# Kernel optimization log

Measured on AMD Instinct MI355X. Metric: run time of the kernel, lower is better.

Reference implementation:

```python
import jax, jax.numpy as jnp
import numpy as np

N_NODES = 100000
N_EDGES = 1000000
N_GRAPHS = 2048
IN_DIM, HIDDEN, OUT_DIM = 5, 64, 128


def setup_inputs() -> dict:
    key = jax.random.key(0)
    ks = jax.random.split(key, 12)
    x = jax.random.normal(ks[0], (N_NODES, IN_DIM), dtype=jnp.float32)
    edge_index = jax.random.randint(ks[1], (2, N_EDGES), 0, N_NODES, dtype=jnp.int64)
    batch = jnp.sort(jax.random.randint(ks[2], (N_NODES,), 0, N_GRAPHS, dtype=jnp.int64))
    def lin(k, fan_in, fan_out):
        bound = 1.0 / np.sqrt(fan_in)
        kw, kb = jax.random.split(k)
        W = jax.random.uniform(kw, (fan_in, fan_out), jnp.float32, -bound, bound)
        b = jax.random.uniform(kb, (fan_out,), jnp.float32, -bound, bound)
        return W, b
    W1, b1 = lin(ks[3], IN_DIM, HIDDEN)
    W2, b2 = lin(ks[4], HIDDEN, HIDDEN)
    W3, b3 = lin(ks[5], HIDDEN, HIDDEN)
    W4, b4 = lin(ks[6], HIDDEN, OUT_DIM)
    return {"x": x, "edge_index": edge_index, "batch": batch,
            "W1": W1, "b1": b1, "W2": W2, "b2": b2,
            "W3": W3, "b3": b3, "W4": W4, "b4": b4}


def _gcn_conv(x, W, b, src, dst, norm, n):
    # h = x W; message from src, scaled by symmetric norm, scattered to dst
    h = x @ W                                   # [N, F]
    msg = h[src] * norm[:, None]                # [E+N, F] gather
    agg = jax.ops.segment_sum(msg, dst, num_segments=n)  # scatter-add
    return agg + b


def reference(x, edge_index, batch, W1, b1, W2, b2, W3, b3, W4, b4):
    n = x.shape[0]
    loop = jnp.arange(n, dtype=edge_index.dtype)
    # GCN with self-loops: src -> dst aggregation, D^-1/2 A_hat D^-1/2 norm
    src = jnp.concatenate([edge_index[0], loop])
    dst = jnp.concatenate([edge_index[1], loop])
    deg = jax.ops.segment_sum(jnp.ones_like(dst, dtype=x.dtype), dst, num_segments=n)
    dinv = jnp.where(deg > 0, jax.lax.rsqrt(jnp.maximum(deg, 1.0)), 0.0)
    norm = dinv[src] * dinv[dst]                # [E+N]

    h = jax.nn.relu(_gcn_conv(x, W1, b1, src, dst, norm, n))
    h = jax.nn.relu(_gcn_conv(h, W2, b2, src, dst, norm, n))

    # global mean pool per graph
    sums = jax.ops.segment_sum(h, batch, num_segments=N_GRAPHS)      # [G, F]
    cnts = jax.ops.segment_sum(jnp.ones((n,), h.dtype), batch, num_segments=N_GRAPHS)
    pooled = sums / jnp.maximum(cnts, 1.0)[:, None]

    # MLP head
    z = jax.nn.relu(pooled @ W3 + b3)
    return z @ W4 + b4
```

## Files before the change

### kernel.cpp

```cpp
#include <hip/hip_runtime.h>
#include <hip/hip_fp16.h>

#define N_NODES  100000
#define N_EDGES  1000000
#define N_GRAPHS 2048
#define IN_DIM   5
#define HIDDEN   64
#define OUT_DIM  128
#define CAP      32
#define NA       512
#define PART     256
#define NBIN     391
#define LSTR     72

typedef _Float16 f16x8 __attribute__((ext_vector_type(8)));
typedef float    f32x4 __attribute__((ext_vector_type(4)));

__global__ void k_hist(const int* __restrict__ dst, int* __restrict__ histT) {
    __shared__ int h[NBIN];
    int t = threadIdx.x, b = blockIdx.x;
    for (int i = t; i < NBIN; i += 256) h[i] = 0;
    __syncthreads();
    for (int e = b * 256 + t; e < N_EDGES; e += NA * 256)
        atomicAdd(&h[dst[e] >> 8], 1);
    __syncthreads();
    for (int i = t; i < NBIN; i += 256) histT[i * NA + b] = h[i];
}

__global__ void k_scanA(int* __restrict__ histT, int* __restrict__ total) {
    __shared__ int s[2][256];
    int bin = blockIdx.x, t = threadIdx.x;
    int* col = histT + bin * NA;
    int v0 = col[2 * t], v1 = col[2 * t + 1];
    int pair = v0 + v1;
    int cur = 0;
    s[0][t] = pair;
    __syncthreads();
    for (int off = 1; off < 256; off <<= 1) {
        int nv = s[cur][t] + ((t >= off) ? s[cur][t - off] : 0);
        s[cur ^ 1][t] = nv;
        cur ^= 1;
        __syncthreads();
    }
    int incl = s[cur][t];
    int excl = incl - pair;
    col[2 * t]     = excl;
    col[2 * t + 1] = excl + v0;
    if (t == 255) total[bin] = incl;
}

__global__ void k_scanB(const int* __restrict__ total, int* __restrict__ binBase) {
    __shared__ int s[2][512];
    int t = threadIdx.x;
    int v = (t < NBIN) ? total[t] : 0;
    int cur = 0;
    s[0][t] = v;
    __syncthreads();
    for (int off = 1; off < 512; off <<= 1) {
        int nv = s[cur][t] + ((t >= off) ? s[cur][t - off] : 0);
        s[cur ^ 1][t] = nv;
        cur ^= 1;
        __syncthreads();
    }
    if (t < NBIN) binBase[t] = s[cur][t] - v;
    if (t == NBIN - 1) binBase[NBIN] = s[cur][t];
}

__global__ void k_part(const int* __restrict__ src, const int* __restrict__ dst,
                       const int* __restrict__ histT, const int* __restrict__ binBase,
                       int* __restrict__ epart) {
    __shared__ int off[NBIN];
    int t = threadIdx.x, b = blockIdx.x;
    for (int i = t; i < NBIN; i += 256)
        off[i] = binBase[i] + histT[i * NA + b];
    __syncthreads();
    for (int e = b * 256 + t; e < N_EDGES; e += NA * 256) {
        int d = dst[e];
        int pos = atomicAdd(&off[d >> 8], 1);
        epart[pos] = ((d & (PART - 1)) << 17) | src[e];
    }
}

__global__ void __launch_bounds__(256) k_build(
        const int* __restrict__ epart, const int* __restrict__ binBase,
        const float* __restrict__ x, int* __restrict__ cnt, int* __restrict__ bkt,
        float* __restrict__ dinv, __half* __restrict__ xs) {
    __shared__ int lcnt[PART];
    __shared__ int lrows[PART * CAP];
    int t = threadIdx.x, b = blockIdx.x;
    int base = b * PART;
    for (int i = t; i < PART; i += 256) lcnt[i] = 0;
    __syncthreads();
    int estart = binBase[b], eend = binBase[b + 1];
    for (int i = estart + t; i < eend; i += 256) {
        int ed = epart[i];
        int ln = ed >> 17;
        int c = atomicAdd(&lcnt[ln], 1);
        if (c < CAP) lrows[ln * CAP + c] = ed & 0x1FFFF;
    }
    __syncthreads();
    int gbase = base * CAP;
    int lim = min(PART * CAP, N_NODES * CAP - gbase);
    for (int i = t; i < lim; i += 256) bkt[gbase + i] = lrows[i];
    for (int n = t; n < PART; n += 256) {
        int g = base + n;
        if (g < N_NODES) {
            int c = lcnt[n];
            cnt[g] = c;
            float d = rsqrtf(1.0f + (float)c);
            dinv[g] = d;
#pragma unroll
            for (int k = 0; k < 8; k++)
                xs[(size_t)g * 8 + k] =
                    __float2half((k < IN_DIM) ? x[g * IN_DIM + k] * d : 0.0f);
        }
    }
}

__global__ void __launch_bounds__(256) k_g5l12(
        const int* __restrict__ cnt, const int* __restrict__ bkt,
        const __half* __restrict__ xs,
        const float* __restrict__ W1, const float* __restrict__ b1,
        const float* __restrict__ W2, const float* __restrict__ dinv,
        __half* __restrict__ hs2h) {
    __shared__ _Float16 lh1[64 * LSTR];
    __shared__ _Float16 lw2[64 * LSTR];
    __shared__ float la5[64][8];
    int tid = threadIdx.x;
    int w = tid >> 6, l = tid & 63;
    int nodeBase = blockIdx.x * 64;

#pragma unroll
    for (int i = 0; i < 16; i++) {
        int idx = tid + i * 256;
        int k = idx >> 6, n = idx & 63;
        lw2[n * LSTR + k] = (_Float16)W2[k * HIDDEN + n];
    }

    {
        int g4 = l >> 2, l4 = l & 3;
        int ln = w * 16 + g4;
        int g = nodeBase + ln;
        float accx = 0.f, accy = 0.f;
        if (g < N_NODES) {
            const __half2* XH = (const __half2*)xs;
            int len = min(cnt[g], CAP);
            const int* row = bkt + (size_t)g * CAP;
            float2 self = __half22float2(XH[(size_t)g * 4 + l4]);
            accx = self.x; accy = self.y;
            for (int e = 0; e < len; e++) {
                int s = row[e];
                float2 v = __half22float2(XH[(size_t)s * 4 + l4]);
                accx += v.x; accy += v.y;
            }
            float d = dinv[g];
            accx *= d; accy *= d;
        }
        la5[ln][l4 * 2]     = accx;
        la5[ln][l4 * 2 + 1] = accy;
    }

    int f = l;
    for (int i = 0; i < 16; i++) {
        int ln = w * 16 + i;
        float t1 = b1[f];
#pragma unroll
        for (int k = 0; k < IN_DIM; k++)
            t1 += la5[ln][k] * W1[k * HIDDEN + f];
        lh1[ln * LSTR + f] = (_Float16)fmaxf(t1, 0.f);
    }
    __syncthreads();

    int quad = l >> 4, m16 = l & 15;
    f32x4 acc0 = {0.f, 0.f, 0.f, 0.f};
    f32x4 acc1 = {0.f, 0.f, 0.f, 0.f};
    f32x4 acc2 = {0.f, 0.f, 0.f, 0.f};
    f32x4 acc3 = {0.f, 0.f, 0.f, 0.f};
#pragma unroll
    for (int kc = 0; kc < 2; kc++) {
        f16x8 a = *(const f16x8*)&lh1[(w * 16 + m16) * LSTR + kc * 32 + quad * 8];
        f16x8 b0 = *(const f16x8*)&lw2[(0 * 16 + m16) * LSTR + kc * 32 + quad * 8];
        f16x8 b1f = *(const f16x8*)&lw2[(1 * 16 + m16) * LSTR + kc * 32 + quad * 8];
        f16x8 b2 = *(const f16x8*)&lw2[(2 * 16 + m16) * LSTR + kc * 32 + quad * 8];
        f16x8 b3 = *(const f16x8*)&lw2[(3 * 16 + m16) * LSTR + kc * 32 + quad * 8];
        acc0 = __builtin_amdgcn_mfma_f32_16x16x32_f16(a, b0, acc0, 0, 0, 0);
        acc1 = __builtin_amdgcn_mfma_f32_16x16x32_f16(a, b1f, acc1, 0, 0, 0);
        acc2 = __builtin_amdgcn_mfma_f32_16x16x32_f16(a, b2, acc2, 0, 0, 0);
        acc3 = __builtin_amdgcn_mfma_f32_16x16x32_f16(a, b3, acc3, 0, 0, 0);
    }
#pragma unroll
    for (int i = 0; i < 4; i++) {
        int g = nodeBase + w * 16 + quad * 4 + i;
        if (g >= N_NODES) continue;
        float dv = dinv[g];
        __half* row = hs2h + (size_t)g * HIDDEN + m16;
        row[0]  = __float2half(acc0[i] * dv);
        row[16] = __float2half(acc1[i] * dv);
        row[32] = __float2half(acc2[i] * dv);
        row[48] = __float2half(acc3[i] * dv);
    }
}

__global__ void __launch_bounds__(256) k_g2head(
        const int* __restrict__ cnt, const int* __restrict__ bkt,
        const __half* __restrict__ hs2h, const float* __restrict__ dinv,
        const int* __restrict__ batch, const float* __restrict__ b2,
        const float* __restrict__ W3, const float* __restrict__ b3,
        const float* __restrict__ W4, const float* __restrict__ b4,
        float* __restrict__ out) {
    __shared__ int range[2];
    __shared__ float4 pool4[4][16];
    __shared__ float p[HIDDEN];
    __shared__ float z[HIDDEN];
    int g = blockIdx.x, tid = threadIdx.x;
    int w = tid >> 6, lane = tid & 63;
    int g16 = lane >> 4, l16 = lane & 15;

    if (tid < 2) {
        int v = g + tid;
        int lo = 0, hi = N_NODES;
        while (lo < hi) {
            int m = (lo + hi) >> 1;
            if (batch[m] < v) lo = m + 1; else hi = m;
        }
        range[tid] = lo;
    }
    __syncthreads();
    int s = range[0], e = range[1];

    const float2* H8 = (const float2*)hs2h;
    float4 b2v = ((const float4*)b2)[l16];
    float4 acc = make_float4(0.f, 0.f, 0.f, 0.f);
    for (int node = s + w * 4 + g16; node < e; node += 16) {
        int len = min(cnt[node], CAP);
        const int* row = bkt + (size_t)node * CAP;
        float ax = 0.f, ay = 0.f, az = 0.f, aw = 0.f;
        float bxx = 0.f, bby = 0.f, bzz = 0.f, bww = 0.f;
        float cx = 0.f, cy = 0.f, cz = 0.f, cw = 0.f;
        float dx = 0.f, dy = 0.f, dz = 0.f, dw = 0.f;
        int idx = 0;
        for (; idx + 3 < len; idx += 4) {
            int s0 = row[idx], s1 = row[idx + 1], s2 = row[idx + 2], s3 = row[idx + 3];
            float2 r0 = H8[(size_t)s0 * 16 + l16];
            float2 r1 = H8[(size_t)s1 * 16 + l16];
            float2 r2 = H8[(size_t)s2 * 16 + l16];
            float2 r3 = H8[(size_t)s3 * 16 + l16];
            const __half2* h0 = (const __half2*)&r0;
            const __half2* h1 = (const __half2*)&r1;
            const __half2* h2 = (const __half2*)&r2;
            const __half2* h3 = (const __half2*)&r3;
            float2 u0 = __half22float2(h0[0]), u1 = __half22float2(h0[1]);
            float2 v0 = __half22float2(h1[0]), v1 = __half22float2(h1[1]);
            float2 q0 = __half22float2(h2[0]), q1 = __half22float2(h2[1]);
            float2 t0 = __half22float2(h3[0]), t1 = __half22float2(h3[1]);
            ax += u0.x; ay += u0.y; az += u1.x; aw += u1.y;
            bxx += v0.x; bby += v0.y; bzz += v1.x; bww += v1.y;
            cx += q0.x; cy += q0.y; cz += q1.x; cw += q1.y;
            dx += t0.x; dy += t0.y; dz += t1.x; dw += t1.y;
        }
        for (; idx < len; idx++) {
            int s0 = row[idx];
            float2 r0 = H8[(size_t)s0 * 16 + l16];
            const __half2* h0 = (const __half2*)&r0;
            float2 u0 = __half22float2(h0[0]), u1 = __half22float2(h0[1]);
            ax += u0.x; ay += u0.y; az += u1.x; aw += u1.y;
        }
        float2 rs = H8[(size_t)node * 16 + l16];
        const __half2* hsp = (const __half2*)&rs;
        float2 s0f = __half22float2(hsp[0]), s1f = __half22float2(hsp[1]);
        float d = dinv[node];
        float ox = (ax + bxx + cx + dx + s0f.x) * d;
        float oy = (ay + bby + cy + dy + s0f.y) * d;
        float oz = (az + bzz + cz + dz + s1f.x) * d;
        float ow = (aw + bww + cw + dw + s1f.y) * d;
        acc.x += fmaxf(ox + b2v.x, 0.f);
        acc.y += fmaxf(oy + b2v.y, 0.f);
        acc.z += fmaxf(oz + b2v.z, 0.f);
        acc.w += fmaxf(ow + b2v.w, 0.f);
    }
    acc.x += __shfl_xor(acc.x, 16); acc.y += __shfl_xor(acc.y, 16);
    acc.z += __shfl_xor(acc.z, 16); acc.w += __shfl_xor(acc.w, 16);
    acc.x += __shfl_xor(acc.x, 32); acc.y += __shfl_xor(acc.y, 32);
    acc.z += __shfl_xor(acc.z, 32); acc.w += __shfl_xor(acc.w, 32);
    if (g16 == 0) pool4[w][l16] = acc;
    __syncthreads();
    if (tid < 16) {
        float4 a0 = pool4[0][tid], a1 = pool4[1][tid];
        float4 a2 = pool4[2][tid], a3 = pool4[3][tid];
        float inv = 1.0f / fmaxf((float)(e - s), 1.0f);
        ((float4*)p)[tid] = make_float4((a0.x + a1.x + a2.x + a3.x) * inv,
                                        (a0.y + a1.y + a2.y + a3.y) * inv,
                                        (a0.z + a1.z + a2.z + a3.z) * inv,
                                        (a0.w + a1.w + a2.w + a3.w) * inv);
    }
    __syncthreads();
    if (tid < HIDDEN) {
        float t = b3[tid];
#pragma unroll 8
        for (int k = 0; k < HIDDEN; k++) t += p[k] * W3[k * HIDDEN + tid];
        z[tid] = fmaxf(t, 0.f);
    }
    __syncthreads();
    if (tid < OUT_DIM) {
        float t = b4[tid];
#pragma unroll 8
        for (int k = 0; k < HIDDEN; k++) t += z[k] * W4[k * OUT_DIM + tid];
        out[(size_t)g * OUT_DIM + tid] = t;
    }
}

extern "C" void kernel_launch(void* const* d_in, const int* in_sizes, int n_in,
                              void* d_out, int out_size, void* d_ws, size_t ws_size,
                              hipStream_t stream) {
    const float* x  = (const float*)d_in[0];
    const int*   ei = (const int*)d_in[1];
    const int*   batch = (const int*)d_in[2];
    const float* W1 = (const float*)d_in[3];
    const float* b1 = (const float*)d_in[4];
    const float* W2 = (const float*)d_in[5];
    const float* b2 = (const float*)d_in[6];
    const float* W3 = (const float*)d_in[7];
    const float* b3 = (const float*)d_in[8];
    const float* W4 = (const float*)d_in[9];
    const float* b4 = (const float*)d_in[10];
    float* out = (float*)d_out;

    const int* src = ei;
    const int* dst = ei + N_EDGES;

    int*   histT   = (int*)d_ws;
    int*   total   = histT + (size_t)NBIN * NA;
    int*   binBase = total + NBIN;
    int*   cnt     = binBase + NBIN + 1;
    int*   bkt     = cnt + N_NODES;
    float* dinv    = (float*)(bkt + (size_t)N_NODES * CAP);
    __half* hs2h   = (__half*)(dinv + N_NODES);
    float* big     = (float*)(hs2h + (size_t)N_NODES * HIDDEN);
    __half* xs     = (__half*)big;
    int*   epart   = (int*)(big + (size_t)N_NODES * 16);

    k_hist<<<NA, 256, 0, stream>>>(dst, histT);
    k_scanA<<<NBIN, 256, 0, stream>>>(histT, total);
    k_scanB<<<1, 512, 0, stream>>>(total, binBase);
    k_part<<<NA, 256, 0, stream>>>(src, dst, histT, binBase, epart);
    k_build<<<NBIN, 256, 0, stream>>>(epart, binBase, x, cnt, bkt, dinv, xs);

    k_g5l12<<<(N_NODES + 63) / 64, 256, 0, stream>>>(cnt, bkt, xs, W1, b1, W2,
                                                     dinv, hs2h);
    k_g2head<<<N_GRAPHS, 256, 0, stream>>>(cnt, bkt, hs2h, dinv, batch, b2,
                                           W3, b3, W4, b4, out);
}
```

Before: 179.6 us.

## Split layer-2 aggregation into node-parallel pooling kernel and separate MLP head

Replaces the per-graph fused aggregation+head kernel with a node-block-parallel kernel that gathers 16-byte rows per lane and pools into shared-memory per-graph slots, flushing them to a global pooled buffer with atomics. A separate head kernel then runs the MLP on four graphs per block. The pooled buffer is zeroed inside the partition kernel, and the layer-1 gather loop gains a 4-way unrolled int4 index load. This removes the load imbalance and the low occupancy of one block per graph, at the cost of float atomics, run-to-run nondeterminism in the sums and one extra launch.

```diff
diff --git a/kernel.cpp b/kernel.cpp
--- a/kernel.cpp
+++ b/kernel.cpp
@@ -12,6 +12,8 @@
 #define PART     256
 #define NBIN     391
 #define LSTR     72
+#define NPB      64
+#define POOLG    16
 
 typedef _Float16 f16x8 __attribute__((ext_vector_type(8)));
 typedef float    f32x4 __attribute__((ext_vector_type(4)));
@@ -68,9 +70,11 @@
 
 __global__ void k_part(const int* __restrict__ src, const int* __restrict__ dst,
                        const int* __restrict__ histT, const int* __restrict__ binBase,
-                       int* __restrict__ epart) {
+                       int* __restrict__ epart, float* __restrict__ pooled) {
     __shared__ int off[NBIN];
     int t = threadIdx.x, b = blockIdx.x;
+    for (int i = b * 256 + t; i < N_GRAPHS * HIDDEN; i += NA * 256)
+        pooled[i] = 0.f;
     for (int i = t; i < NBIN; i += 256)
         off[i] = binBase[i] + histT[i * NA + b];
     __syncthreads();
@@ -148,7 +152,17 @@
             const int* row = bkt + (size_t)g * CAP;
             float2 self = __half22float2(XH[(size_t)g * 4 + l4]);
             accx = self.x; accy = self.y;
-            for (int e = 0; e < len; e++) {
+            int e = 0;
+            for (; e + 4 <= len; e += 4) {
+                int4 ii = *(const int4*)&row[e];
+                float2 v0 = __half22float2(XH[(size_t)ii.x * 4 + l4]);
+                float2 v1 = __half22float2(XH[(size_t)ii.y * 4 + l4]);
+                float2 v2 = __half22float2(XH[(size_t)ii.z * 4 + l4]);
+                float2 v3 = __half22float2(XH[(size_t)ii.w * 4 + l4]);
+                accx += (v0.x + v1.x) + (v2.x + v3.x);
+                accy += (v0.y + v1.y) + (v2.y + v3.y);
+            }
+            for (; e < len; e++) {
                 int s = row[e];
                 float2 v = __half22float2(XH[(size_t)s * 4 + l4]);
                 accx += v.x; accy += v.y;
@@ -201,23 +215,125 @@
     }
 }
 
-__global__ void __launch_bounds__(256) k_g2head(
+__global__ void __launch_bounds__(256) k_g2agg(
         const int* __restrict__ cnt, const int* __restrict__ bkt,
         const __half* __restrict__ hs2h, const float* __restrict__ dinv,
         const int* __restrict__ batch, const float* __restrict__ b2,
+        float* __restrict__ pooled) {
+    __shared__ float pool[POOLG][HIDDEN];
+    __shared__ int gbase_s;
+    int tid = threadIdx.x;
+    int grp = tid >> 3, l8 = tid & 7;
+    int base = blockIdx.x * NPB;
+    for (int i = tid; i < POOLG * HIDDEN; i += 256) ((float*)pool)[i] = 0.f;
+    if (tid == 0) gbase_s = batch[base];
+    __syncthreads();
+    int gbase = gbase_s;
+    const float4* H16 = (const float4*)hs2h;
+    float4 b2a = ((const float4*)b2)[l8 * 2];
+    float4 b2b = ((const float4*)b2)[l8 * 2 + 1];
+
+#define ACCA(r) { const __half2* hp_ = (const __half2*)&(r);               \
+        float2 u0_ = __half22float2(hp_[0]), u1_ = __half22float2(hp_[1]); \
+        float2 u2_ = __half22float2(hp_[2]), u3_ = __half22float2(hp_[3]); \
+        a0 += u0_.x; a1 += u0_.y; a2 += u1_.x; a3 += u1_.y;                \
+        a4 += u2_.x; a5 += u2_.y; a6 += u3_.x; a7 += u3_.y; }
+#define ACCC(r) { const __half2* hp_ = (const __half2*)&(r);               \
+        float2 u0_ = __half22float2(hp_[0]), u1_ = __half22float2(hp_[1]); \
+        float2 u2_ = __half22float2(hp_[2]), u3_ = __half22float2(hp_[3]); \
+        c0 += u0_.x; c1 += u0_.y; c2 += u1_.x; c3 += u1_.y;                \
+        c4 += u2_.x; c5 += u2_.y; c6 += u3_.x; c7 += u3_.y; }
+
+    for (int ln = grp; ln < NPB; ln += 32) {
+        int node = base + ln;
+        if (node >= N_NODES) break;
+        int len = min(cnt[node], CAP);
+        const int* row = bkt + (size_t)node * CAP;
+        float a0 = 0.f, a1 = 0.f, a2 = 0.f, a3 = 0.f;
+        float a4 = 0.f, a5 = 0.f, a6 = 0.f, a7 = 0.f;
+        float c0 = 0.f, c1 = 0.f, c2 = 0.f, c3 = 0.f;
+        float c4 = 0.f, c5 = 0.f, c6 = 0.f, c7 = 0.f;
+        int e = 0;
+        for (; e + 8 <= len; e += 8) {
+            int4 i0 = *(const int4*)&row[e];
+            int4 i1 = *(const int4*)&row[e + 4];
+            float4 r0 = H16[(size_t)i0.x * 8 + l8];
+            float4 r1 = H16[(size_t)i0.y * 8 + l8];
+            float4 r2 = H16[(size_t)i0.z * 8 + l8];
+            float4 r3 = H16[(size_t)i0.w * 8 + l8];
+            float4 r4 = H16[(size_t)i1.x * 8 + l8];
+            float4 r5 = H16[(size_t)i1.y * 8 + l8];
+            float4 r6 = H16[(size_t)i1.z * 8 + l8];
+            float4 r7 = H16[(size_t)i1.w * 8 + l8];
+            ACCA(r0); ACCC(r1); ACCA(r2); ACCC(r3);
+            ACCA(r4); ACCC(r5); ACCA(r6); ACCC(r7);
+        }
+        if (e + 4 <= len) {
+            int4 i0 = *(const int4*)&row[e];
+            float4 r0 = H16[(size_t)i0.x * 8 + l8];
+            float4 r1 = H16[(size_t)i0.y * 8 + l8];
+            float4 r2 = H16[(size_t)i0.z * 8 + l8];
+            float4 r3 = H16[(size_t)i0.w * 8 + l8];
+            ACCA(r0); ACCC(r1); ACCA(r2); ACCC(r3);
+            e += 4;
+        }
+        for (; e < len; e++) {
+            float4 r0 = H16[(size_t)row[e] * 8 + l8];
+            ACCA(r0);
+        }
+        {
+            float4 rs = H16[(size_t)node * 8 + l8];
+            ACCA(rs);
+        }
+        float d = dinv[node];
+        float h0 = fmaxf((a0 + c0) * d + b2a.x, 0.f);
+        float h1 = fmaxf((a1 + c1) * d + b2a.y, 0.f);
+        float h2 = fmaxf((a2 + c2) * d + b2a.z, 0.f);
+        float h3 = fmaxf((a3 + c3) * d + b2a.w, 0.f);
+        float h4 = fmaxf((a4 + c4) * d + b2b.x, 0.f);
+        float h5 = fmaxf((a5 + c5) * d + b2b.y, 0.f);
+        float h6 = fmaxf((a6 + c6) * d + b2b.z, 0.f);
+        float h7 = fmaxf((a7 + c7) * d + b2b.w, 0.f);
+        int gslot = batch[node] - gbase;
+        if ((unsigned)gslot < POOLG) {
+            float* pp = &pool[gslot][l8 * 8];
+            atomicAdd(pp + 0, h0); atomicAdd(pp + 1, h1);
+            atomicAdd(pp + 2, h2); atomicAdd(pp + 3, h3);
+            atomicAdd(pp + 4, h4); atomicAdd(pp + 5, h5);
+            atomicAdd(pp + 6, h6); atomicAdd(pp + 7, h7);
+        } else {
+            float* pp = &pooled[(size_t)batch[node] * HIDDEN + l8 * 8];
+            atomicAdd(pp + 0, h0); atomicAdd(pp + 1, h1);
+            atomicAdd(pp + 2, h2); atomicAdd(pp + 3, h3);
+            atomicAdd(pp + 4, h4); atomicAdd(pp + 5, h5);
+            atomicAdd(pp + 6, h6); atomicAdd(pp + 7, h7);
+        }
+    }
+    __syncthreads();
+    int last = min(base + NPB, N_NODES) - 1;
+    int span = batch[last] - gbase + 1;
+    if (span > POOLG) span = POOLG;
+    for (int i = tid; i < span * HIDDEN; i += 256) {
+        float v = ((const float*)pool)[i];
+        if (v != 0.f)
+            atomicAdd(&pooled[(size_t)gbase * HIDDEN + i], v);
+    }
+#undef ACCA
+#undef ACCC
+}
+
+__global__ void __launch_bounds__(256) k_head(
+        const float* __restrict__ pooled, const int* __restrict__ batch,
         const float* __restrict__ W3, const float* __restrict__ b3,
         const float* __restrict__ W4, const float* __restrict__ b4,
         float* __restrict__ out) {
-    __shared__ int range[2];
-    __shared__ float4 pool4[4][16];
-    __shared__ float p[HIDDEN];
-    __shared__ float z[HIDDEN];
-    int g = blockIdx.x, tid = threadIdx.x;
-    int w = tid >> 6, lane = tid & 63;
-    int g16 = lane >> 4, l16 = lane & 15;
-
-    if (tid < 2) {
-        int v = g + tid;
+    __shared__ float p[4][HIDDEN];
+    __shared__ float z[4][HIDDEN];
+    __shared__ int range[5];
+    int tid = threadIdx.x;
+    int g0 = blockIdx.x * 4;
+    if (tid < 5) {
+        int v = g0 + tid;
         int lo = 0, hi = N_NODES;
         while (lo < hi) {
             int m = (lo + hi) >> 1;
@@ -226,86 +342,26 @@
         range[tid] = lo;
     }
     __syncthreads();
-    int s = range[0], e = range[1];
-
-    const float2* H8 = (const float2*)hs2h;
-    float4 b2v = ((const float4*)b2)[l16];
-    float4 acc = make_float4(0.f, 0.f, 0.f, 0.f);
-    for (int node = s + w * 4 + g16; node < e; node += 16) {
-        int len = min(cnt[node], CAP);
-        const int* row = bkt + (size_t)node * CAP;
-        float ax = 0.f, ay = 0.f, az = 0.f, aw = 0.f;
-        float bxx = 0.f, bby = 0.f, bzz = 0.f, bww = 0.f;
-        float cx = 0.f, cy = 0.f, cz = 0.f, cw = 0.f;
-        float dx = 0.f, dy = 0.f, dz = 0.f, dw = 0.f;
-        int idx = 0;
-        for (; idx + 3 < len; idx += 4) {
-            int s0 = row[idx], s1 = row[idx + 1], s2 = row[idx + 2], s3 = row[idx + 3];
-            float2 r0 = H8[(size_t)s0 * 16 + l16];
-            float2 r1 = H8[(size_t)s1 * 16 + l16];
-            float2 r2 = H8[(size_t)s2 * 16 + l16];
-            float2 r3 = H8[(size_t)s3 * 16 + l16];
-            const __half2* h0 = (const __half2*)&r0;
-            const __half2* h1 = (const __half2*)&r1;
-            const __half2* h2 = (const __half2*)&r2;
-            const __half2* h3 = (const __half2*)&r3;
-            float2 u0 = __half22float2(h0[0]), u1 = __half22float2(h0[1]);
-            float2 v0 = __half22float2(h1[0]), v1 = __half22float2(h1[1]);
-            float2 q0 = __half22float2(h2[0]), q1 = __half22float2(h2[1]);
-            float2 t0 = __half22float2(h3[0]), t1 = __half22float2(h3[1]);
-            ax += u0.x; ay += u0.y; az += u1.x; aw += u1.y;
-            bxx += v0.x; bby += v0.y; bzz += v1.x; bww += v1.y;
-            cx += q0.x; cy += q0.y; cz += q1.x; cw += q1.y;
-            dx += t0.x; dy += t0.y; dz += t1.x; dw += t1.y;
-        }
-        for (; idx < len; idx++) {
-            int s0 = row[idx];
-            float2 r0 = H8[(size_t)s0 * 16 + l16];
-            const __half2* h0 = (const __half2*)&r0;
-            float2 u0 = __half22float2(h0[0]), u1 = __half22float2(h0[1]);
-            ax += u0.x; ay += u0.y; az += u1.x; aw += u1.y;
-        }
-        float2 rs = H8[(size_t)node * 16 + l16];
-        const __half2* hsp = (const __half2*)&rs;
-        float2 s0f = __half22float2(hsp[0]), s1f = __half22float2(hsp[1]);
-        float d = dinv[node];
-        float ox = (ax + bxx + cx + dx + s0f.x) * d;
-        float oy = (ay + bby + cy + dy + s0f.y) * d;
-        float oz = (az + bzz + cz + dz + s1f.x) * d;
-        float ow = (aw + bww + cw + dw + s1f.y) * d;
-        acc.x += fmaxf(ox + b2v.x, 0.f);
-        acc.y += fmaxf(oy + b2v.y, 0.f);
-        acc.z += fmaxf(oz + b2v.z, 0.f);
-        acc.w += fmaxf(ow + b2v.w, 0.f);
-    }
-    acc.x += __shfl_xor(acc.x, 16); acc.y += __shfl_xor(acc.y, 16);
-    acc.z += __shfl_xor(acc.z, 16); acc.w += __shfl_xor(acc.w, 16);
-    acc.x += __shfl_xor(acc.x, 32); acc.y += __shfl_xor(acc.y, 32);
-    acc.z += __shfl_xor(acc.z, 32); acc.w += __shfl_xor(acc.w, 32);
-    if (g16 == 0) pool4[w][l16] = acc;
-    __syncthreads();
-    if (tid < 16) {
-        float4 a0 = pool4[0][tid], a1 = pool4[1][tid];
-        float4 a2 = pool4[2][tid], a3 = pool4[3][tid];
-        float inv = 1.0f / fmaxf((float)(e - s), 1.0f);
-        ((float4*)p)[tid] = make_float4((a0.x + a1.x + a2.x + a3.x) * inv,
-                                        (a0.y + a1.y + a2.y + a3.y) * inv,
-                                        (a0.z + a1.z + a2.z + a3.z) * inv,
-                                        (a0.w + a1.w + a2.w + a3.w) * inv);
-    }
-    __syncthreads();
-    if (tid < HIDDEN) {
-        float t = b3[tid];
+    {
+        int gi = tid >> 6, f = tid & 63;
+        float c = (float)(range[gi + 1] - range[gi]);
+        p[gi][f] = pooled[(size_t)(g0 + gi) * HIDDEN + f] / fmaxf(c, 1.f);
+    }
+    __syncthreads();
+    {
+        int gi = tid >> 6, f = tid & 63;
+        float t = b3[f];
 #pragma unroll 8
-        for (int k = 0; k < HIDDEN; k++) t += p[k] * W3[k * HIDDEN + tid];
-        z[tid] = fmaxf(t, 0.f);
-    }
-    __syncthreads();
-    if (tid < OUT_DIM) {
-        float t = b4[tid];
+        for (int k = 0; k < HIDDEN; k++) t += p[gi][k] * W3[k * HIDDEN + f];
+        z[gi][f] = fmaxf(t, 0.f);
+    }
+    __syncthreads();
+    for (int i = tid; i < 4 * OUT_DIM; i += 256) {
+        int gi = i >> 7, o = i & 127;
+        float t = b4[o];
 #pragma unroll 8
-        for (int k = 0; k < HIDDEN; k++) t += z[k] * W4[k * OUT_DIM + tid];
-        out[(size_t)g * OUT_DIM + tid] = t;
+        for (int k = 0; k < HIDDEN; k++) t += z[gi][k] * W4[k * OUT_DIM + o];
+        out[(size_t)(g0 + gi) * OUT_DIM + o] = t;
     }
 }
 
@@ -328,25 +384,32 @@
     const int* src = ei;
     const int* dst = ei + N_EDGES;
 
-    int*   histT   = (int*)d_ws;
-    int*   total   = histT + (size_t)NBIN * NA;
-    int*   binBase = total + NBIN;
-    int*   cnt     = binBase + NBIN + 1;
-    int*   bkt     = cnt + N_NODES;
-    float* dinv    = (float*)(bkt + (size_t)N_NODES * CAP);
-    __half* hs2h   = (__half*)(dinv + N_NODES);
-    float* big     = (float*)(hs2h + (size_t)N_NODES * HIDDEN);
-    __half* xs     = (__half*)big;
-    int*   epart   = (int*)(big + (size_t)N_NODES * 16);
+    char* wp = (char*)d_ws;
+    auto carve = [&](size_t bytes) -> void* {
+        void* p = (void*)wp;
+        wp += (bytes + 255) & ~(size_t)255;
+        return p;
+    };
+    int*    histT   = (int*)carve((size_t)NBIN * NA * sizeof(int));
+    int*    total   = (int*)carve((size_t)NBIN * sizeof(int));
+    int*    binBase = (int*)carve((size_t)(NBIN + 1) * sizeof(int));
+    int*    cnt     = (int*)carve((size_t)N_NODES * sizeof(int));
+    int*    bkt     = (int*)carve((size_t)N_NODES * CAP * sizeof(int));
+    float*  dinv    = (float*)carve((size_t)N_NODES * sizeof(float));
+    __half* hs2h    = (__half*)carve((size_t)N_NODES * HIDDEN * sizeof(__half));
+    __half* xs      = (__half*)carve((size_t)N_NODES * 8 * sizeof(__half));
+    int*    epart   = (int*)carve((size_t)N_EDGES * sizeof(int));
+    float*  pooled  = (float*)carve((size_t)N_GRAPHS * HIDDEN * sizeof(float));
 
     k_hist<<<NA, 256, 0, stream>>>(dst, histT);
     k_scanA<<<NBIN, 256, 0, stream>>>(histT, total);
     k_scanB<<<1, 512, 0, stream>>>(total, binBase);
-    k_part<<<NA, 256, 0, stream>>>(src, dst, histT, binBase, epart);
+    k_part<<<NA, 256, 0, stream>>>(src, dst, histT, binBase, epart, pooled);
     k_build<<<NBIN, 256, 0, stream>>>(epart, binBase, x, cnt, bkt, dinv, xs);
 
     k_g5l12<<<(N_NODES + 63) / 64, 256, 0, stream>>>(cnt, bkt, xs, W1, b1, W2,
                                                      dinv, hs2h);
-    k_g2head<<<N_GRAPHS, 256, 0, stream>>>(cnt, bkt, hs2h, dinv, batch, b2,
-                                           W3, b3, W4, b4, out);
-}
+    k_g2agg<<<(N_NODES + NPB - 1) / NPB, 256, 0, stream>>>(cnt, bkt, hs2h, dinv,
+                                                           batch, b2, pooled);
+    k_head<<<N_GRAPHS / 4, 256, 0, stream>>>(pooled, batch, W3, b3, W4, b4, out);
+}
```

Result: slower. 188.5 us (+5.0%).
